# Kernel optimization log

Measured on AMD Instinct MI355X. Metric: run time of the kernel, lower is better.

Reference implementation:

```python
import jax, jax.numpy as jnp
import numpy as np

B, P, D = 64, 128, 128   # clouds, points per cloud, vec_dim
N = B * P                # 8192 nodes
EPS = 1e-5


def _complete_graph_edges():
    # knn_graph with k == total node count => complete graph per cloud (no self loops)
    i = np.arange(P)
    ii, jj = np.meshgrid(i, i, indexing='ij')
    m = ii != jj
    li, lj = ii[m], jj[m]                      # [P*(P-1)] local pairs
    off = (np.arange(B) * P)[:, None]          # cloud offsets
    src = (off + li[None, :]).reshape(-1)      # neighbor index
    dst = (off + lj[None, :]).reshape(-1)      # center index
    return jnp.asarray(src, jnp.int32), jnp.asarray(dst, jnp.int32)


def setup_inputs() -> dict:
    key = jax.random.key(0)
    ks = jax.random.split(key, 4)
    src, dst = _complete_graph_edges()
    return {
        'x': jax.random.normal(ks[0], (N, D), jnp.float32),
        'xyz': jax.random.normal(ks[1], (N, 3), jnp.float32),
        'W_xyz': jax.random.normal(ks[2], (3, D), jnp.float32) * 0.1,
        'bn_gamma': jnp.ones((D,), jnp.float32),
        'bn_beta': jnp.zeros((D,), jnp.float32),
        'W1': jax.random.normal(ks[3], (D, D), jnp.float32) * 0.05,
        'b1': jnp.zeros((D,), jnp.float32),
        'ln_gamma': jnp.ones((D,), jnp.float32),
        'ln_beta': jnp.zeros((D,), jnp.float32),
        'src': src,
        'dst': dst,
    }


def reference(x, xyz, W_xyz, bn_gamma, bn_beta, W1, b1, ln_gamma, ln_beta, src, dst):
    n = x.shape[0]
    rela_xyz = xyz[src] - xyz[dst]                         # [E, 3]
    rela_x = x[src] - x[dst]                               # [E, D]
    dist = jnp.sqrt(jnp.sum(rela_xyz * rela_xyz, axis=-1))  # [E]
    w = jnp.exp(-dist)[:, None]                            # [E, 1]

    # weighted linear + relu, pool by src (global_add_pool over node index)
    h1 = jax.nn.relu((w * rela_x) @ W1 + b1)               # [E, D]
    p1 = jax.ops.segment_sum(h1, src, num_segments=n)      # [N, D]
    mu = jnp.mean(p1, axis=-1, keepdims=True)
    var = jnp.var(p1, axis=-1, keepdims=True)
    x = x + ((p1 - mu) / jnp.sqrt(var + EPS)) * ln_gamma + ln_beta

    # xyz projection branch, BatchNorm1d (training-mode batch stats)
    h2 = jax.nn.relu(rela_xyz @ W_xyz)                     # [E, D]
    p2 = jax.ops.segment_sum(h2, src, num_segments=n)      # [N, D]
    bmu = jnp.mean(p2, axis=0)
    bvar = jnp.var(p2, axis=0)
    x = x + ((p2 - bmu) / jnp.sqrt(bvar + EPS)) * bn_gamma + bn_beta
    return x
```

## Files before the change

### kernel.cpp

```cpp
#include <hip/hip_runtime.h>
#include <stdint.h>

#define EPS 1e-5f
#define N_NODES 8192

typedef __attribute__((ext_vector_type(8))) short short8;
typedef __attribute__((ext_vector_type(4))) float floatx4;
typedef __attribute__((ext_vector_type(2))) float floatx2;
typedef __attribute__((ext_vector_type(4))) unsigned short ushortx4;

__device__ __forceinline__ unsigned short f2bf(float f) {
    uint32_t u = __float_as_uint(f);
    u += 0x7FFFu + ((u >> 16) & 1u);
    return (unsigned short)(u >> 16);
}

__global__ __launch_bounds__(256) void prep_kernel(
    const float* __restrict__ x, const float* __restrict__ W1,
    unsigned short* __restrict__ xb, unsigned short* __restrict__ w1t,
    float* __restrict__ stat_ws)
{
    const int bx = blockIdx.x, tid = threadIdx.x;
    if (bx < 1024) {
        const int base = bx * 1024 + tid * 4;
        floatx4 v = *(const floatx4*)(x + base);
        ushortx4 o = { f2bf(v[0]), f2bf(v[1]), f2bf(v[2]), f2bf(v[3]) };
        *(ushortx4*)(xb + base) = o;
    } else {
        const int b2 = bx - 1024;
        const int n = b2 * 8 + (tid >> 5);
        const int k = (tid & 31) * 4;
#pragma unroll
        for (int e = 0; e < 4; ++e)
            w1t[n * 128 + k + e] = f2bf(W1[(k + e) * 128 + n]);
        if (b2 == 0) {
            floatx4 z = {0.f, 0.f, 0.f, 0.f};
            *(floatx4*)(stat_ws + tid * 4) = z;
        }
    }
}

__global__ __launch_bounds__(64) void gemm_y_kernel(
    const unsigned short* __restrict__ xb, const unsigned short* __restrict__ w1t,
    float* __restrict__ y)
{
    const int lane = threadIdx.x;
    const int ml = lane & 15, q = lane >> 4;
    const int rb = blockIdx.x * 16;

    short8 afrag[4];
#pragma unroll
    for (int c = 0; c < 4; ++c)
        afrag[c] = *(const short8*)(xb + (rb + ml) * 128 + c * 32 + q * 8);

#pragma unroll
    for (int nt = 0; nt < 8; ++nt) {
        floatx4 acc = {0.f, 0.f, 0.f, 0.f};
        const int ncol = nt * 16 + ml;
#pragma unroll
        for (int c = 0; c < 4; ++c) {
            short8 b = *(const short8*)(w1t + ncol * 128 + c * 32 + q * 8);
            acc = __builtin_amdgcn_mfma_f32_16x16x32_bf16(afrag[c], b, acc, 0, 0, 0);
        }
#pragma unroll
        for (int r = 0; r < 4; ++r)
            y[(rb + q * 4 + r) * 128 + ncol] = acc[r];
    }
}

__global__ __launch_bounds__(256, 4) void cloud_main_kernel(
    const float* __restrict__ x, const float* __restrict__ xyz,
    const float* __restrict__ W_xyz, const float* __restrict__ b1,
    const float* __restrict__ ln_gamma, const float* __restrict__ ln_beta,
    const float* __restrict__ y_ws, float* __restrict__ p2_ws,
    float* __restrict__ stat_ws, float* __restrict__ out)
{
    __shared__ float s_xyz[512];
    __shared__ float s_w[1024];
    __shared__ float s_red[2048];
    __shared__ float s_p1[1088];
    __shared__ float s_bn[256];
    __shared__ float s_mu[8];
    __shared__ float s_rs[8];

    const int bx = blockIdx.x;
    const int c = bx & 63, s = bx >> 6;
    const int tid = threadIdx.x;
    const int d = tid & 127, h = tid >> 7;
    const int node0 = c * 128;
    const int i0 = s * 8;

    if (tid < 128) {
        const float* p = xyz + (node0 + tid) * 3;
        s_xyz[tid * 4 + 0] = p[0];
        s_xyz[tid * 4 + 1] = p[1];
        s_xyz[tid * 4 + 2] = p[2];
        s_xyz[tid * 4 + 3] = 0.f;
    }
    __syncthreads();

    for (int e = tid; e < 1024; e += 256) {
        const int j = e >> 3, ii = e & 7, ia = i0 + ii;
        float dx = s_xyz[ia * 4]     - s_xyz[j * 4];
        float dy = s_xyz[ia * 4 + 1] - s_xyz[j * 4 + 1];
        float dz = s_xyz[ia * 4 + 2] - s_xyz[j * 4 + 2];
        s_w[j * 8 + ii] = __expf(-sqrtf(dx * dx + dy * dy + dz * dz));
    }
    __syncthreads();

    const float w0 = W_xyz[d], w1c = W_xyz[128 + d], w2c = W_xyz[256 + d];
    const float b1d = b1[d];
    const floatx2 b1v = {b1d, b1d};
    const floatx2 zv2 = {0.f, 0.f};

    floatx2 yi[4], zi[4], a1[4], a2[4];
#pragma unroll
    for (int r = 0; r < 8; ++r) {
        const int ia = i0 + r;
        yi[r >> 1][r & 1] = y_ws[(node0 + ia) * 128 + d];
        zi[r >> 1][r & 1] = s_xyz[ia * 4] * w0 + s_xyz[ia * 4 + 1] * w1c
                          + s_xyz[ia * 4 + 2] * w2c;
        a1[r >> 1][r & 1] = 0.f;
        a2[r >> 1][r & 1] = 0.f;
    }

    const float* yrow = y_ws + (node0 + h * 64) * 128 + d;
    const float* wp = s_w + h * 64 * 8;
    const float* xp = s_xyz + h * 64 * 4;

#pragma unroll 4
    for (int j = 0; j < 64; ++j) {
        const float yj = yrow[j * 128];
        floatx4 xj = *(const floatx4*)(xp + j * 4);
        const float zj = xj[0] * w0 + xj[1] * w1c + xj[2] * w2c;
        floatx4 wa = *(const floatx4*)(wp + j * 8);
        floatx4 wb = *(const floatx4*)(wp + j * 8 + 4);
        const floatx2 yj2 = {yj, yj}, zj2 = {zj, zj};
        floatx2 wlo = {wa[0], wa[1]}, wmd = {wa[2], wa[3]};
        floatx2 wh0 = {wb[0], wb[1]}, wh1 = {wb[2], wb[3]};
        a1[0] += __builtin_elementwise_max(wlo * (yi[0] - yj2) + b1v, zv2);
        a1[1] += __builtin_elementwise_max(wmd * (yi[1] - yj2) + b1v, zv2);
        a1[2] += __builtin_elementwise_max(wh0 * (yi[2] - yj2) + b1v, zv2);
        a1[3] += __builtin_elementwise_max(wh1 * (yi[3] - yj2) + b1v, zv2);
        a2[0] += __builtin_elementwise_max(zi[0] - zj2, zv2);
        a2[1] += __builtin_elementwise_max(zi[1] - zj2, zv2);
        a2[2] += __builtin_elementwise_max(zi[2] - zj2, zv2);
        a2[3] += __builtin_elementwise_max(zi[3] - zj2, zv2);
    }
    __syncthreads();

    if (h == 1) {
#pragma unroll
        for (int r = 0; r < 8; ++r) {
            s_red[r * 128 + d]        = a1[r >> 1][r & 1];
            s_red[1024 + r * 128 + d] = a2[r >> 1][r & 1];
        }
    }
    __syncthreads();

    if (h == 0) {
        const float selfc = fmaxf(b1d, 0.f);
        float bs = 0.f, bq = 0.f;
#pragma unroll
        for (int r = 0; r < 8; ++r) {
            float v1 = a1[r >> 1][r & 1] + s_red[r * 128 + d] - selfc;
            float v2 = a2[r >> 1][r & 1] + s_red[1024 + r * 128 + d];
            a1[r >> 1][r & 1] = v1;
            a2[r >> 1][r & 1] = v2;
            s_p1[r * 136 + d] = v1;
            bs += v2;
            bq += v2 * v2;
        }
        s_bn[d] = bs;
        s_bn[128 + d] = bq;
    }
    __syncthreads();

    {
        const int ii = tid >> 5, sub = tid & 31;
        floatx4 v = *(const floatx4*)(s_p1 + ii * 136 + sub * 4);
        float ps = v[0] + v[1] + v[2] + v[3];
        float pq = v[0] * v[0] + v[1] * v[1] + v[2] * v[2] + v[3] * v[3];
#pragma unroll
        for (int m = 1; m < 32; m <<= 1) {
            ps += __shfl_xor(ps, m, 64);
            pq += __shfl_xor(pq, m, 64);
        }
        if (sub == 0) {
            float mu = ps * (1.f / 128.f);
            float var = pq * (1.f / 128.f) - mu * mu;
            s_mu[ii] = mu;
            s_rs[ii] = rsqrtf(var + EPS);
        }
    }
    if (tid < 128) {
        const int bank = (s & 3) * 256;
        atomicAdd(stat_ws + bank + d,       s_bn[d]);
        atomicAdd(stat_ws + bank + 128 + d, s_bn[128 + d]);
    }
    __syncthreads();

    if (h == 0) {
        const float lng = ln_gamma[d], lnb = ln_beta[d];
#pragma unroll
        for (int r = 0; r < 8; ++r) {
            const int gi = node0 + i0 + r;
            float o = x[gi * 128 + d] + (a1[r >> 1][r & 1] - s_mu[r]) * s_rs[r] * lng + lnb;
            out[gi * 128 + d] = o;
            p2_ws[gi * 128 + d] = a2[r >> 1][r & 1];
        }
    }
}

__global__ __launch_bounds__(256) void finalize_kernel(
    const float* __restrict__ p2_ws, const float* __restrict__ stat_ws,
    const float* __restrict__ bn_gamma, const float* __restrict__ bn_beta,
    float* __restrict__ out)
{
    __shared__ float sA[128], sB[128];
    const int tid = threadIdx.x;
    if (tid < 128) {
        float sm = 0.f, sq = 0.f;
#pragma unroll
        for (int b = 0; b < 4; ++b) {
            sm += stat_ws[b * 256 + tid];
            sq += stat_ws[b * 256 + 128 + tid];
        }
        float mu = sm * (1.f / 8192.f);
        float var = sq * (1.f / 8192.f) - mu * mu;
        float rs = rsqrtf(var + EPS);
        float A = rs * bn_gamma[tid];
        sA[tid] = A;
        sB[tid] = bn_beta[tid] - mu * A;
    }
    __syncthreads();
    const int base = (blockIdx.x * 256 + tid) * 4;
    const int d0 = base & 127;
    floatx4 p2 = *(const floatx4*)(p2_ws + base);
    floatx4 o  = *(const floatx4*)(out + base);
#pragma unroll
    for (int e = 0; e < 4; ++e)
        o[e] += p2[e] * sA[d0 + e] + sB[d0 + e];
    *(floatx4*)(out + base) = o;
}

extern "C" void kernel_launch(void* const* d_in, const int* in_sizes, int n_in,
                              void* d_out, int out_size, void* d_ws, size_t ws_size,
                              hipStream_t stream) {
    const float* x        = (const float*)d_in[0];
    const float* xyz      = (const float*)d_in[1];
    const float* W_xyz    = (const float*)d_in[2];
    const float* bn_gamma = (const float*)d_in[3];
    const float* bn_beta  = (const float*)d_in[4];
    const float* W1       = (const float*)d_in[5];
    const float* b1       = (const float*)d_in[6];
    const float* ln_gamma = (const float*)d_in[7];
    const float* ln_beta  = (const float*)d_in[8];
    float* out = (float*)d_out;

    float* y_ws    = (float*)d_ws;
    float* p2_ws   = y_ws + N_NODES * 128;
    float* stat_ws = p2_ws + N_NODES * 128;
    unsigned short* xb  = (unsigned short*)(stat_ws + 1024);
    unsigned short* w1t = xb + N_NODES * 128;

    prep_kernel<<<1040, 256, 0, stream>>>(x, W1, xb, w1t, stat_ws);
    gemm_y_kernel<<<512, 64, 0, stream>>>(xb, w1t, y_ws);
    cloud_main_kernel<<<1024, 256, 0, stream>>>(x, xyz, W_xyz, b1, ln_gamma, ln_beta,
                                                y_ws, p2_ws, stat_ws, out);
    finalize_kernel<<<1024, 256, 0, stream>>>(p2_ws, stat_ws, bn_gamma, bn_beta, out);
}
```

Before: 113.0 us.

## Precompute pairwise exp-distance weights and padded xyz in prep kernel

```diff
diff --git a/kernel.cpp b/kernel.cpp
--- a/kernel.cpp
+++ b/kernel.cpp
@@ -17,16 +17,19 @@
 
 __global__ __launch_bounds__(256) void prep_kernel(
     const float* __restrict__ x, const float* __restrict__ W1,
+    const float* __restrict__ xyz,
     unsigned short* __restrict__ xb, unsigned short* __restrict__ w1t,
+    float* __restrict__ xyz4, float* __restrict__ w_ws,
     float* __restrict__ stat_ws)
 {
+    __shared__ float sx[512];
     const int bx = blockIdx.x, tid = threadIdx.x;
     if (bx < 1024) {
         const int base = bx * 1024 + tid * 4;
         floatx4 v = *(const floatx4*)(x + base);
         ushortx4 o = { f2bf(v[0]), f2bf(v[1]), f2bf(v[2]), f2bf(v[3]) };
         *(ushortx4*)(xb + base) = o;
-    } else {
+    } else if (bx < 1040) {
         const int b2 = bx - 1024;
         const int n = b2 * 8 + (tid >> 5);
         const int k = (tid & 31) * 4;
@@ -37,6 +40,34 @@
             floatx4 z = {0.f, 0.f, 0.f, 0.f};
             *(floatx4*)(stat_ws + tid * 4) = z;
         }
+    } else if (bx < 1048) {
+        const int node = (bx - 1040) * 1024 + tid * 4;
+#pragma unroll
+        for (int e = 0; e < 4; ++e) {
+            const float* p = xyz + (node + e) * 3;
+            floatx4 v = { p[0], p[1], p[2], 0.f };
+            *(floatx4*)(xyz4 + (node + e) * 4) = v;
+        }
+    } else {
+        const int cc = bx - 1048;
+        if (tid < 128) {
+            const float* p = xyz + (cc * 128 + tid) * 3;
+            sx[tid * 4 + 0] = p[0];
+            sx[tid * 4 + 1] = p[1];
+            sx[tid * 4 + 2] = p[2];
+            sx[tid * 4 + 3] = 0.f;
+        }
+        __syncthreads();
+        const int i = tid & 127, jh = tid >> 7;
+        const float xi0 = sx[i * 4], xi1 = sx[i * 4 + 1], xi2 = sx[i * 4 + 2];
+        float* wdst = w_ws + cc * 16384 + i;
+        for (int jj = 0; jj < 64; ++jj) {
+            const int j = jh * 64 + jj;
+            float dx = xi0 - sx[j * 4];
+            float dy = xi1 - sx[j * 4 + 1];
+            float dz = xi2 - sx[j * 4 + 2];
+            wdst[j * 128] = __expf(-sqrtf(dx * dx + dy * dy + dz * dz));
+        }
     }
 }
 
@@ -69,14 +100,13 @@
 }
 
 __global__ __launch_bounds__(256, 4) void cloud_main_kernel(
-    const float* __restrict__ x, const float* __restrict__ xyz,
-    const float* __restrict__ W_xyz, const float* __restrict__ b1,
+    const float* __restrict__ x, const float* __restrict__ W_xyz,
+    const float* __restrict__ b1,
     const float* __restrict__ ln_gamma, const float* __restrict__ ln_beta,
+    const float* __restrict__ xyz4, const float* __restrict__ w_ws,
     const float* __restrict__ y_ws, float* __restrict__ p2_ws,
     float* __restrict__ stat_ws, float* __restrict__ out)
 {
-    __shared__ float s_xyz[512];
-    __shared__ float s_w[1024];
     __shared__ float s_red[2048];
     __shared__ float s_p1[1088];
     __shared__ float s_bn[256];
@@ -90,64 +120,48 @@
     const int node0 = c * 128;
     const int i0 = s * 8;
 
-    if (tid < 128) {
-        const float* p = xyz + (node0 + tid) * 3;
-        s_xyz[tid * 4 + 0] = p[0];
-        s_xyz[tid * 4 + 1] = p[1];
-        s_xyz[tid * 4 + 2] = p[2];
-        s_xyz[tid * 4 + 3] = 0.f;
-    }
-    __syncthreads();
-
-    for (int e = tid; e < 1024; e += 256) {
-        const int j = e >> 3, ii = e & 7, ia = i0 + ii;
-        float dx = s_xyz[ia * 4]     - s_xyz[j * 4];
-        float dy = s_xyz[ia * 4 + 1] - s_xyz[j * 4 + 1];
-        float dz = s_xyz[ia * 4 + 2] - s_xyz[j * 4 + 2];
-        s_w[j * 8 + ii] = __expf(-sqrtf(dx * dx + dy * dy + dz * dz));
-    }
-    __syncthreads();
-
     const float w0 = W_xyz[d], w1c = W_xyz[128 + d], w2c = W_xyz[256 + d];
     const float b1d = b1[d];
     const floatx2 b1v = {b1d, b1d};
     const floatx2 zv2 = {0.f, 0.f};
 
+    const float* __restrict__ wrow  = w_ws + c * 16384 + i0;
+    const float* __restrict__ xzrow = xyz4 + node0 * 4;
+    const float* __restrict__ yrow  = y_ws + node0 * 128 + d;
+
     floatx2 yi[4], zi[4], a1[4], a2[4];
 #pragma unroll
     for (int r = 0; r < 8; ++r) {
         const int ia = i0 + r;
-        yi[r >> 1][r & 1] = y_ws[(node0 + ia) * 128 + d];
-        zi[r >> 1][r & 1] = s_xyz[ia * 4] * w0 + s_xyz[ia * 4 + 1] * w1c
-                          + s_xyz[ia * 4 + 2] * w2c;
+        yi[r >> 1][r & 1] = yrow[ia * 128];
+        const float* xi = xzrow + ia * 4;
+        zi[r >> 1][r & 1] = xi[0] * w0 + xi[1] * w1c + xi[2] * w2c;
         a1[r >> 1][r & 1] = 0.f;
         a2[r >> 1][r & 1] = 0.f;
     }
 
-    const float* yrow = y_ws + (node0 + h * 64) * 128 + d;
-    const float* wp = s_w + h * 64 * 8;
-    const float* xp = s_xyz + h * 64 * 4;
-
+    const int jbase = h * 64;
 #pragma unroll 4
-    for (int j = 0; j < 64; ++j) {
+    for (int jj = 0; jj < 64; ++jj) {
+        const int j = jbase + jj;
         const float yj = yrow[j * 128];
-        floatx4 xj = *(const floatx4*)(xp + j * 4);
+        floatx4 xj = *(const floatx4*)(xzrow + j * 4);
         const float zj = xj[0] * w0 + xj[1] * w1c + xj[2] * w2c;
-        floatx4 wa = *(const floatx4*)(wp + j * 8);
-        floatx4 wb = *(const floatx4*)(wp + j * 8 + 4);
+        const float* wp = wrow + j * 128;
+        floatx2 w01 = { wp[0], wp[1] };
+        floatx2 w23 = { wp[2], wp[3] };
+        floatx2 w45 = { wp[4], wp[5] };
+        floatx2 w67 = { wp[6], wp[7] };
         const floatx2 yj2 = {yj, yj}, zj2 = {zj, zj};
-        floatx2 wlo = {wa[0], wa[1]}, wmd = {wa[2], wa[3]};
-        floatx2 wh0 = {wb[0], wb[1]}, wh1 = {wb[2], wb[3]};
-        a1[0] += __builtin_elementwise_max(wlo * (yi[0] - yj2) + b1v, zv2);
-        a1[1] += __builtin_elementwise_max(wmd * (yi[1] - yj2) + b1v, zv2);
-        a1[2] += __builtin_elementwise_max(wh0 * (yi[2] - yj2) + b1v, zv2);
-        a1[3] += __builtin_elementwise_max(wh1 * (yi[3] - yj2) + b1v, zv2);
+        a1[0] += __builtin_elementwise_max(w01 * (yi[0] - yj2) + b1v, zv2);
+        a1[1] += __builtin_elementwise_max(w23 * (yi[1] - yj2) + b1v, zv2);
+        a1[2] += __builtin_elementwise_max(w45 * (yi[2] - yj2) + b1v, zv2);
+        a1[3] += __builtin_elementwise_max(w67 * (yi[3] - yj2) + b1v, zv2);
         a2[0] += __builtin_elementwise_max(zi[0] - zj2, zv2);
         a2[1] += __builtin_elementwise_max(zi[1] - zj2, zv2);
         a2[2] += __builtin_elementwise_max(zi[2] - zj2, zv2);
         a2[3] += __builtin_elementwise_max(zi[3] - zj2, zv2);
     }
-    __syncthreads();
 
     if (h == 1) {
 #pragma unroll
@@ -263,10 +277,12 @@
     float* stat_ws = p2_ws + N_NODES * 128;
     unsigned short* xb  = (unsigned short*)(stat_ws + 1024);
     unsigned short* w1t = xb + N_NODES * 128;
-
-    prep_kernel<<<1040, 256, 0, stream>>>(x, W1, xb, w1t, stat_ws);
+    float* xyz4 = (float*)(w1t + 128 * 128);
+    float* w_ws = xyz4 + N_NODES * 4;
+
+    prep_kernel<<<1112, 256, 0, stream>>>(x, W1, xyz, xb, w1t, xyz4, w_ws, stat_ws);
     gemm_y_kernel<<<512, 64, 0, stream>>>(xb, w1t, y_ws);
-    cloud_main_kernel<<<1024, 256, 0, stream>>>(x, xyz, W_xyz, b1, ln_gamma, ln_beta,
-                                                y_ws, p2_ws, stat_ws, out);
+    cloud_main_kernel<<<1024, 256, 0, stream>>>(x, W_xyz, b1, ln_gamma, ln_beta,
+                                                xyz4, w_ws, y_ws, p2_ws, stat_ws, out);
     finalize_kernel<<<1024, 256, 0, stream>>>(p2_ws, stat_ws, bn_gamma, bn_beta, out);
 }
```

After: 128.6 us. 13.8% more time.

## Precompute xyz projection in GEMM kernel and interleave with y values

Applied to the files above, without the earlier changes.

```diff
diff --git a/kernel.cpp b/kernel.cpp
--- a/kernel.cpp
+++ b/kernel.cpp
@@ -17,8 +17,9 @@
 
 __global__ __launch_bounds__(256) void prep_kernel(
     const float* __restrict__ x, const float* __restrict__ W1,
+    const float* __restrict__ xyz,
     unsigned short* __restrict__ xb, unsigned short* __restrict__ w1t,
-    float* __restrict__ stat_ws)
+    float* __restrict__ xyz4, float* __restrict__ stat_ws)
 {
     const int bx = blockIdx.x, tid = threadIdx.x;
     if (bx < 1024) {
@@ -26,7 +27,7 @@
         floatx4 v = *(const floatx4*)(x + base);
         ushortx4 o = { f2bf(v[0]), f2bf(v[1]), f2bf(v[2]), f2bf(v[3]) };
         *(ushortx4*)(xb + base) = o;
-    } else {
+    } else if (bx < 1040) {
         const int b2 = bx - 1024;
         const int n = b2 * 8 + (tid >> 5);
         const int k = (tid & 31) * 4;
@@ -37,12 +38,21 @@
             floatx4 z = {0.f, 0.f, 0.f, 0.f};
             *(floatx4*)(stat_ws + tid * 4) = z;
         }
-    }
-}
-
-__global__ __launch_bounds__(64) void gemm_y_kernel(
+    } else {
+        const int node = (bx - 1040) * 1024 + tid * 4;
+#pragma unroll
+        for (int e = 0; e < 4; ++e) {
+            const float* p = xyz + (node + e) * 3;
+            floatx4 v = { p[0], p[1], p[2], 0.f };
+            *(floatx4*)(xyz4 + (node + e) * 4) = v;
+        }
+    }
+}
+
+__global__ __launch_bounds__(64) void gemm_yz_kernel(
     const unsigned short* __restrict__ xb, const unsigned short* __restrict__ w1t,
-    float* __restrict__ y)
+    const float* __restrict__ xyz4, const float* __restrict__ W_xyz,
+    float* __restrict__ yz)
 {
     const int lane = threadIdx.x;
     const int ml = lane & 15, q = lane >> 4;
@@ -53,27 +63,37 @@
     for (int c = 0; c < 4; ++c)
         afrag[c] = *(const short8*)(xb + (rb + ml) * 128 + c * 32 + q * 8);
 
+    floatx4 xn[4];
+#pragma unroll
+    for (int r = 0; r < 4; ++r)
+        xn[r] = *(const floatx4*)(xyz4 + (rb + q * 4 + r) * 4);
+
 #pragma unroll
     for (int nt = 0; nt < 8; ++nt) {
+        const int ncol = nt * 16 + ml;
+        const float wx0 = W_xyz[ncol], wx1 = W_xyz[128 + ncol], wx2 = W_xyz[256 + ncol];
         floatx4 acc = {0.f, 0.f, 0.f, 0.f};
-        const int ncol = nt * 16 + ml;
 #pragma unroll
         for (int c = 0; c < 4; ++c) {
             short8 b = *(const short8*)(w1t + ncol * 128 + c * 32 + q * 8);
             acc = __builtin_amdgcn_mfma_f32_16x16x32_bf16(afrag[c], b, acc, 0, 0, 0);
         }
 #pragma unroll
-        for (int r = 0; r < 4; ++r)
-            y[(rb + q * 4 + r) * 128 + ncol] = acc[r];
+        for (int r = 0; r < 4; ++r) {
+            const int node = rb + q * 4 + r;
+            float zv = xn[r][0] * wx0 + xn[r][1] * wx1 + xn[r][2] * wx2;
+            floatx2 st = { acc[r], zv };
+            *(floatx2*)(yz + node * 256 + 2 * ncol) = st;
+        }
     }
 }
 
 __global__ __launch_bounds__(256, 4) void cloud_main_kernel(
-    const float* __restrict__ x, const float* __restrict__ xyz,
-    const float* __restrict__ W_xyz, const float* __restrict__ b1,
+    const float* __restrict__ x, const float* __restrict__ b1,
     const float* __restrict__ ln_gamma, const float* __restrict__ ln_beta,
-    const float* __restrict__ y_ws, float* __restrict__ p2_ws,
-    float* __restrict__ stat_ws, float* __restrict__ out)
+    const float* __restrict__ xyz4, const float* __restrict__ yz,
+    float* __restrict__ p2_ws, float* __restrict__ stat_ws,
+    float* __restrict__ out)
 {
     __shared__ float s_xyz[512];
     __shared__ float s_w[1024];
@@ -90,13 +110,8 @@
     const int node0 = c * 128;
     const int i0 = s * 8;
 
-    if (tid < 128) {
-        const float* p = xyz + (node0 + tid) * 3;
-        s_xyz[tid * 4 + 0] = p[0];
-        s_xyz[tid * 4 + 1] = p[1];
-        s_xyz[tid * 4 + 2] = p[2];
-        s_xyz[tid * 4 + 3] = 0.f;
-    }
+    if (tid < 128)
+        *(floatx4*)(s_xyz + tid * 4) = *(const floatx4*)(xyz4 + (node0 + tid) * 4);
     __syncthreads();
 
     for (int e = tid; e < 1024; e += 256) {
@@ -108,46 +123,42 @@
     }
     __syncthreads();
 
-    const float w0 = W_xyz[d], w1c = W_xyz[128 + d], w2c = W_xyz[256 + d];
     const float b1d = b1[d];
     const floatx2 b1v = {b1d, b1d};
     const floatx2 zv2 = {0.f, 0.f};
 
+    const float* __restrict__ yzrow = yz + node0 * 256 + 2 * d;
+
     floatx2 yi[4], zi[4], a1[4], a2[4];
 #pragma unroll
     for (int r = 0; r < 8; ++r) {
-        const int ia = i0 + r;
-        yi[r >> 1][r & 1] = y_ws[(node0 + ia) * 128 + d];
-        zi[r >> 1][r & 1] = s_xyz[ia * 4] * w0 + s_xyz[ia * 4 + 1] * w1c
-                          + s_xyz[ia * 4 + 2] * w2c;
+        floatx2 v = *(const floatx2*)(yzrow + (i0 + r) * 256);
+        yi[r >> 1][r & 1] = v[0];
+        zi[r >> 1][r & 1] = v[1];
         a1[r >> 1][r & 1] = 0.f;
         a2[r >> 1][r & 1] = 0.f;
     }
 
-    const float* yrow = y_ws + (node0 + h * 64) * 128 + d;
-    const float* wp = s_w + h * 64 * 8;
-    const float* xp = s_xyz + h * 64 * 4;
+    const float* __restrict__ yzp = yzrow + h * 64 * 256;
+    const float* __restrict__ wp = s_w + h * 64 * 8;
 
 #pragma unroll 4
-    for (int j = 0; j < 64; ++j) {
-        const float yj = yrow[j * 128];
-        floatx4 xj = *(const floatx4*)(xp + j * 4);
-        const float zj = xj[0] * w0 + xj[1] * w1c + xj[2] * w2c;
-        floatx4 wa = *(const floatx4*)(wp + j * 8);
-        floatx4 wb = *(const floatx4*)(wp + j * 8 + 4);
-        const floatx2 yj2 = {yj, yj}, zj2 = {zj, zj};
-        floatx2 wlo = {wa[0], wa[1]}, wmd = {wa[2], wa[3]};
-        floatx2 wh0 = {wb[0], wb[1]}, wh1 = {wb[2], wb[3]};
-        a1[0] += __builtin_elementwise_max(wlo * (yi[0] - yj2) + b1v, zv2);
-        a1[1] += __builtin_elementwise_max(wmd * (yi[1] - yj2) + b1v, zv2);
-        a1[2] += __builtin_elementwise_max(wh0 * (yi[2] - yj2) + b1v, zv2);
-        a1[3] += __builtin_elementwise_max(wh1 * (yi[3] - yj2) + b1v, zv2);
+    for (int jj = 0; jj < 64; ++jj) {
+        floatx2 yzj = *(const floatx2*)(yzp + jj * 256);
+        floatx4 wa = *(const floatx4*)(wp + jj * 8);
+        floatx4 wb = *(const floatx4*)(wp + jj * 8 + 4);
+        const floatx2 yj2 = {yzj[0], yzj[0]}, zj2 = {yzj[1], yzj[1]};
+        floatx2 w01 = {wa[0], wa[1]}, w23 = {wa[2], wa[3]};
+        floatx2 w45 = {wb[0], wb[1]}, w67 = {wb[2], wb[3]};
+        a1[0] += __builtin_elementwise_max(w01 * (yi[0] - yj2) + b1v, zv2);
+        a1[1] += __builtin_elementwise_max(w23 * (yi[1] - yj2) + b1v, zv2);
+        a1[2] += __builtin_elementwise_max(w45 * (yi[2] - yj2) + b1v, zv2);
+        a1[3] += __builtin_elementwise_max(w67 * (yi[3] - yj2) + b1v, zv2);
         a2[0] += __builtin_elementwise_max(zi[0] - zj2, zv2);
         a2[1] += __builtin_elementwise_max(zi[1] - zj2, zv2);
         a2[2] += __builtin_elementwise_max(zi[2] - zj2, zv2);
         a2[3] += __builtin_elementwise_max(zi[3] - zj2, zv2);
     }
-    __syncthreads();
 
     if (h == 1) {
 #pragma unroll
@@ -258,15 +269,16 @@
     const float* ln_beta  = (const float*)d_in[8];
     float* out = (float*)d_out;
 
-    float* y_ws    = (float*)d_ws;
-    float* p2_ws   = y_ws + N_NODES * 128;
+    float* yz_ws   = (float*)d_ws;
+    float* p2_ws   = yz_ws + N_NODES * 256;
     float* stat_ws = p2_ws + N_NODES * 128;
     unsigned short* xb  = (unsigned short*)(stat_ws + 1024);
     unsigned short* w1t = xb + N_NODES * 128;
-
-    prep_kernel<<<1040, 256, 0, stream>>>(x, W1, xb, w1t, stat_ws);
-    gemm_y_kernel<<<512, 64, 0, stream>>>(xb, w1t, y_ws);
-    cloud_main_kernel<<<1024, 256, 0, stream>>>(x, xyz, W_xyz, b1, ln_gamma, ln_beta,
-                                                y_ws, p2_ws, stat_ws, out);
+    float* xyz4 = (float*)(w1t + 128 * 128);
+
+    prep_kernel<<<1048, 256, 0, stream>>>(x, W1, xyz, xb, w1t, xyz4, stat_ws);
+    gemm_yz_kernel<<<512, 64, 0, stream>>>(xb, w1t, xyz4, W_xyz, yz_ws);
+    cloud_main_kernel<<<1024, 256, 0, stream>>>(x, b1, ln_gamma, ln_beta,
+                                                xyz4, yz_ws, p2_ws, stat_ws, out);
     finalize_kernel<<<1024, 256, 0, stream>>>(p2_ws, stat_ws, bn_gamma, bn_beta, out);
 }
```

New measurement: 114.3 us. About the same (+1.1%).
